# Kernel tuning notes

Measured on AMD Instinct MI355X. Metric: run time of the kernel, lower is better.

Reference implementation:

```python
import jax, jax.numpy as jnp
import numpy as np

B, S, E, H = 2, 2048, 2048, 16
D = E // H  # head_dim = 128
MASKED_BIAS = -1e9


def setup_inputs() -> dict:
    key = jax.random.key(0)
    ks = jax.random.split(key, 5)
    scale = 0.02
    return {
        "hidden_states": jax.random.normal(ks[0], (B, S, E), dtype=jnp.float32),
        "Wq": jax.random.normal(ks[1], (E, E), dtype=jnp.float32) * scale,
        "Wk": jax.random.normal(ks[2], (E, E), dtype=jnp.float32) * scale,
        "Wv": jax.random.normal(ks[3], (E, E), dtype=jnp.float32) * scale,
        "Wo": jax.random.normal(ks[4], (E, E), dtype=jnp.float32) * scale,
        "bo": jnp.zeros((E,), dtype=jnp.float32),
    }


def reference(hidden_states, Wq, Wk, Wv, Wo, bo):
    x = hidden_states
    # torch Linear: y = x @ W.T (no bias for q/k/v)
    q = jnp.einsum("bse,fe->bsf", x, Wq).reshape(B, S, H, D).transpose(0, 2, 1, 3)
    k = jnp.einsum("bse,fe->bsf", x, Wk).reshape(B, S, H, D).transpose(0, 2, 1, 3)
    v = jnp.einsum("bse,fe->bsf", x, Wv).reshape(B, S, H, D).transpose(0, 2, 1, 3)
    # GPT-Neo: NO 1/sqrt(d) scaling, attention computed in fp32
    scores = jnp.einsum("bhqd,bhkd->bhqk", q.astype(jnp.float32), k.astype(jnp.float32))
    causal = jnp.tril(jnp.ones((S, S), dtype=bool))[None, None]
    scores = jnp.where(causal, scores, jnp.float32(MASKED_BIAS))
    weights = jax.nn.softmax(scores, axis=-1).astype(v.dtype)
    attn = jnp.einsum("bhqk,bhkd->bhqd", weights, v)
    attn = attn.transpose(0, 2, 1, 3).reshape(B, S, E)
    out = jnp.einsum("bse,fe->bsf", attn, Wo) + bo
    return out
```

## Files before the change

### kernel.cpp

```cpp
#include <hip/hip_runtime.h>
#include <stdint.h>
#include <stddef.h>

#define Bd 2
#define Sd 2048
#define Ed 2048
#define Hd 16
#define Dd 128

typedef unsigned short u16;
typedef _Float16 f16;
typedef __attribute__((ext_vector_type(8))) _Float16 half8;
typedef __attribute__((ext_vector_type(4))) float f32x4;

__device__ __forceinline__ u16 f2h(float f) {
  f16 h = (f16)f; return __builtin_bit_cast(u16, h);
}
__device__ __forceinline__ void gll16(const void* g, void* lds) {
  __builtin_amdgcn_global_load_lds(
      (const __attribute__((address_space(1))) void*)g,
      (__attribute__((address_space(3))) void*)lds, 16, 0, 0);
}
template<int C> __device__ __forceinline__ float dppmv(float x) {
  return __builtin_bit_cast(float,
      __builtin_amdgcn_update_dpp(0, __builtin_bit_cast(int, x), C, 0xF, 0xF, false));
}
__device__ __forceinline__ float rmax16(float x) {
  x = fmaxf(x, dppmv<0x121>(x)); x = fmaxf(x, dppmv<0x122>(x));
  x = fmaxf(x, dppmv<0x124>(x)); x = fmaxf(x, dppmv<0x128>(x));
  return x;
}
__device__ __forceinline__ float rsum16(float x) {
  x += dppmv<0x121>(x); x += dppmv<0x122>(x);
  x += dppmv<0x124>(x); x += dppmv<0x128>(x);
  return x;
}
#define MFMA(a,b,c) __builtin_amdgcn_mfma_f32_16x16x32_f16((a),(b),(c),0,0,0)

#define BARRIER() do { __builtin_amdgcn_s_barrier(); __builtin_amdgcn_sched_barrier(0); } while (0)
#define LGKM(n) do { asm volatile("s_waitcnt lgkmcnt(" #n ")" ::: "memory"); __builtin_amdgcn_sched_barrier(0); } while (0)
#define VMCNT(n) do { asm volatile("s_waitcnt vmcnt(" #n ")" ::: "memory"); __builtin_amdgcn_sched_barrier(0); } while (0)

__global__ void k_cvt5(const float* __restrict__ x,
                       const float* __restrict__ Wq, const float* __restrict__ Wk,
                       const float* __restrict__ Wv, const float* __restrict__ Wo,
                       u16* __restrict__ xh, u16* __restrict__ wq, u16* __restrict__ wk,
                       u16* __restrict__ wv, u16* __restrict__ wo) {
  const int stride = gridDim.x * blockDim.x;
  for (int i = blockIdx.x * blockDim.x + threadIdx.x; i < 6291456; i += stride) {
    const float* s; u16* d; int j;
    if (i < 2097152) { s = x; d = xh; j = i; }
    else {
      const int t = (i - 2097152) >> 20;
      j = (i - 2097152) & 1048575;
      s = (t == 0) ? Wq : (t == 1) ? Wk : (t == 2) ? Wv : Wo;
      d = (t == 0) ? wq : (t == 1) ? wk : (t == 2) ? wv : wo;
    }
    const float4 v = ((const float4*)s)[j];
    ((ushort4*)d)[j] = make_ushort4(f2h(v.x), f2h(v.y), f2h(v.z), f2h(v.w));
  }
}

__global__ __launch_bounds__(512, 2) void gemm_qk(
    const u16* __restrict__ xh,
    const u16* __restrict__ wq, const u16* __restrict__ wk,
    u16* __restrict__ Qf, u16* __restrict__ Kf) {
  constexpr int NT = 32;
  __shared__ __align__(16) char smem[131072];
  const int lin = blockIdx.x;
  const int z = lin >> 7;
  const int rr = lin & 127;
  const int n0 = (rr & 7) * 256;
  const int m0 = (rr >> 3) * 256;
  const u16* wgt = z ? wk : wq;
  u16* oq = z ? Kf : Qf;
  const int tid = threadIdx.x, wv = tid >> 6, ln = tid & 63;
  const int wvm = wv >> 2, wvn = wv & 3;

  auto stgA = [&](int tt, int par) {
    if (tt >= NT) return;
    const int kin = tt << 6;
    const int c = tt & 1;
    const int r8 = ln >> 3, cc = ((ln & 7) ^ r8) * 16;
#pragma unroll
    for (int e = 0; e < 2; ++e) {
      const int ch = e * 8 + wv;
      const int trow = (par + (ch >> 3) * 2) * 64 + (ch & 7) * 8;
      gll16((const char*)xh + (size_t)(m0 + trow + r8) * 4096 + (size_t)kin * 2 + cc,
            smem + c * 65536 + trow * 128);
    }
  };
  auto stgB = [&](int tt, int n2) {
    if (tt >= NT) return;
    const int kin = tt << 6;
    const int c = tt & 1;
    const int r8 = ln >> 3, cc = ((ln & 7) ^ r8) * 16;
#pragma unroll
    for (int e = 0; e < 2; ++e) {
      const int ch = e * 8 + wv;
      const int trow = (ch >> 2) * 64 + n2 * 32 + (ch & 3) * 8;
      gll16((const char*)wgt + (size_t)(n0 + trow + r8) * 4096 + (size_t)kin * 2 + cc,
            smem + c * 65536 + 32768 + trow * 128);
    }
  };
  auto ldAh = [&](int c, int h, half8 (*a)[2]) {
#pragma unroll
    for (int mm = 0; mm < 4; ++mm) {
      const int row = wvm * 128 + h * 64 + mm * 16 + (ln & 15);
#pragma unroll
      for (int s = 0; s < 2; ++s) {
        const int cb = (s * 64 + (ln >> 4) * 16) ^ ((row & 7) << 4);
        a[mm][s] = *(const half8*)(smem + c * 65536 + row * 128 + cb);
      }
    }
  };
  auto ldBh = [&](int c, int n2, half8 (*b)[2]) {
#pragma unroll
    for (int nn = 0; nn < 2; ++nn) {
      const int row = wvn * 64 + (n2 * 2 + nn) * 16 + (ln & 15);
#pragma unroll
      for (int s = 0; s < 2; ++s) {
        const int cb = (s * 64 + (ln >> 4) * 16) ^ ((row & 7) << 4);
        b[nn][s] = *(const half8*)(smem + c * 65536 + 32768 + row * 128 + cb);
      }
    }
  };

  const f32x4 fz = {0.f, 0.f, 0.f, 0.f};
  f32x4 acc[8][4];
#pragma unroll
  for (int mm = 0; mm < 8; ++mm)
#pragma unroll
    for (int nn = 0; nn < 4; ++nn) acc[mm][nn] = fz;

#define QUAD(MB, NB, AA, BB)                                                    \
  do {                                                                          \
    __builtin_amdgcn_s_setprio(1);                                              \
    _Pragma("unroll")                                                           \
    for (int mm = 0; mm < 4; ++mm)                                              \
      _Pragma("unroll")                                                         \
      for (int nn = 0; nn < 2; ++nn) {                                          \
        acc[MB + mm][NB + nn] = MFMA(AA[mm][0], BB[nn][0], acc[MB + mm][NB + nn]); \
        acc[MB + mm][NB + nn] = MFMA(AA[mm][1], BB[nn][1], acc[MB + mm][NB + nn]); \
      }                                                                         \
    __builtin_amdgcn_s_setprio(0);                                              \
  } while (0)

  stgA(0, 0); stgA(0, 1); stgB(0, 0); stgB(0, 1);
  stgA(1, 0); stgB(1, 0); stgB(1, 1);
  VMCNT(6);
  BARRIER();

  for (int w = 0; w < NT; ++w) {
    const int c = w & 1;
    half8 a[4][2], b0[2][2], b1[2][2];
    ldAh(c, 0, a);
    ldBh(c, 0, b0);
    stgA(w + 1, 1);
    BARRIER(); LGKM(0);
    QUAD(0, 0, a, b0);
    BARRIER();
    ldBh(c, 1, b1);
    stgA(w + 2, 0);
    BARRIER(); LGKM(0);
    QUAD(0, 2, a, b1);
    BARRIER();
    ldAh(c, 1, a);
    stgB(w + 2, 0);
    BARRIER(); LGKM(0);
    QUAD(4, 0, a, b0);
    BARRIER();
    stgB(w + 2, 1);
    BARRIER();
    QUAD(4, 2, a, b1);
    if (w + 2 < NT) { VMCNT(6); } else { VMCNT(0); }
    BARRIER();
  }
#undef QUAD

#pragma unroll
  for (int mm = 0; mm < 8; ++mm)
#pragma unroll
    for (int nn = 0; nn < 4; ++nn)
#pragma unroll
      for (int r4 = 0; r4 < 4; ++r4) {
        const int mg = m0 + wvm * 128 + mm * 16 + (ln >> 4) * 4 + r4;
        const int f = n0 + wvn * 64 + nn * 16 + (ln & 15);
        const int b = mg >> 11, s = mg & (Sd - 1);
        const int h = f >> 7, d = f & (Dd - 1);
        oq[(((size_t)b * Hd + h) * Sd + s) * Dd + d] = f2h(acc[mm][nn][r4]);
      }
}

template<int MODE>
__global__ __launch_bounds__(512, 2) void gemm1(
    const u16* __restrict__ Ap, const u16* __restrict__ Bp,
    const float* __restrict__ bias, u16* __restrict__ ob, float* __restrict__ of) {
  constexpr int NT = 32;
  __shared__ __align__(16) char smem[98304];
  const int bid = blockIdx.x;
  const int n0 = (bid & 7) * 256;
  const int m0 = (bid >> 3) * 128;
  const int tid = threadIdx.x, wv = tid >> 6, ln = tid & 63;
  const int wvm = wv >> 2, wvn = wv & 3;

  auto stageA = [&](int tt, int c) {
    const int kin = tt << 6;
#pragma unroll
    for (int i = 0; i < 2; ++i) {
      const int l2 = i * 8192 + wv * 1024 + ln * 16;
      const int row = l2 >> 7, cb = l2 & 127;
      const int gc = cb ^ ((row & 7) << 4);
      gll16((const char*)Ap + (size_t)(m0 + row) * 4096 + (size_t)kin * 2 + gc,
            smem + c * 49152 + i * 8192 + wv * 1024);
    }
  };
  auto stageB = [&](int tt, int c) {
    const int kin = tt << 6;
#pragma unroll
    for (int i = 0; i < 4; ++i) {
      const int l2 = i * 8192 + wv * 1024 + ln * 16;
      const int row = l2 >> 7, cb = l2 & 127;
      const int gc = cb ^ ((row & 7) << 4);
      gll16((const char*)Bp + (size_t)(n0 + row) * 4096 + (size_t)kin * 2 + gc,
            smem + c * 49152 + 16384 + i * 8192 + wv * 1024);
    }
  };
  auto ldA = [&](int c, int s, half8* af) {
#pragma unroll
    for (int mm = 0; mm < 4; ++mm) {
      const int row = wvm * 64 + mm * 16 + (ln & 15);
      const int cb = (s * 64 + (ln >> 4) * 16) ^ ((row & 7) << 4);
      af[mm] = *(const half8*)(smem + c * 49152 + row * 128 + cb);
    }
  };
  auto ldB = [&](int c, int s, int p, half8* bf) {
#pragma unroll
    for (int j = 0; j < 2; ++j) {
      const int row = wvn * 64 + (p * 2 + j) * 16 + (ln & 15);
      const int cb = (s * 64 + (ln >> 4) * 16) ^ ((row & 7) << 4);
      bf[j] = *(const half8*)(smem + c * 49152 + 16384 + row * 128 + cb);
    }
  };

  const f32x4 fz = {0.f, 0.f, 0.f, 0.f};
  f32x4 acc[4][4];
#pragma unroll
  for (int mm = 0; mm < 4; ++mm)
#pragma unroll
    for (int nn = 0; nn < 4; ++nn) acc[mm][nn] = fz;

  stageA(0, 0);
  stageB(0, 0);
  stageA(1, 1);
  VMCNT(2);
  BARRIER();

  for (int t = 0; t < NT; ++t) {
    const int c = t & 1;
    const bool h1 = (t + 1 < NT), h2 = (t + 2 < NT);
    half8 af[4], bf01[2], bf23[2];
    ldA(c, 0, af);
    ldB(c, 0, 0, bf01);
    ldB(c, 0, 1, bf23);
    if (h1) stageB(t + 1, c ^ 1);
    BARRIER();
    LGKM(2);
    __builtin_amdgcn_s_setprio(1);
#pragma unroll
    for (int mm = 0; mm < 4; ++mm) {
      acc[mm][0] = MFMA(af[mm], bf01[0], acc[mm][0]);
      acc[mm][1] = MFMA(af[mm], bf01[1], acc[mm][1]);
    }
    __builtin_amdgcn_s_setprio(0);
    BARRIER();
    LGKM(0);
    __builtin_amdgcn_s_setprio(1);
#pragma unroll
    for (int mm = 0; mm < 4; ++mm) {
      acc[mm][2] = MFMA(af[mm], bf23[0], acc[mm][2]);
      acc[mm][3] = MFMA(af[mm], bf23[1], acc[mm][3]);
    }
    __builtin_amdgcn_s_setprio(0);
    BARRIER();
    ldA(c, 1, af);
    ldB(c, 1, 0, bf01);
    ldB(c, 1, 1, bf23);
    BARRIER();
    LGKM(2);
    __builtin_amdgcn_s_setprio(1);
#pragma unroll
    for (int mm = 0; mm < 4; ++mm) {
      acc[mm][0] = MFMA(af[mm], bf01[0], acc[mm][0]);
      acc[mm][1] = MFMA(af[mm], bf01[1], acc[mm][1]);
    }
    __builtin_amdgcn_s_setprio(0);
    BARRIER();
    if (h2) stageA(t + 2, c);
    LGKM(0);
    __builtin_amdgcn_s_setprio(1);
#pragma unroll
    for (int mm = 0; mm < 4; ++mm) {
      acc[mm][2] = MFMA(af[mm], bf23[0], acc[mm][2]);
      acc[mm][3] = MFMA(af[mm], bf23[1], acc[mm][3]);
    }
    __builtin_amdgcn_s_setprio(0);
    if (h2)      { VMCNT(2); }
    else if (h1) { VMCNT(0); }
    BARRIER();
  }

#pragma unroll
  for (int mm = 0; mm < 4; ++mm)
#pragma unroll
    for (int nn = 0; nn < 4; ++nn) {
      const int f = n0 + wvn * 64 + nn * 16 + (ln & 15);
      float bi = 0.f;
      if (MODE == 1) bi = bias[f];
#pragma unroll
      for (int r4 = 0; r4 < 4; ++r4) {
        const int mg = m0 + wvm * 64 + mm * 16 + (ln >> 4) * 4 + r4;
        if (MODE == 0) {
          const int b = mg >> 11, s = mg & (Sd - 1);
          const int h = f >> 7, d = f & (Dd - 1);
          ob[(((size_t)b * Hd + h) * Sd + s) * Dd + d] = f2h(acc[mm][nn][r4]);
        } else {
          of[(size_t)mg * Ed + f] = acc[mm][nn][r4] + bi;
        }
      }
    }
}

__global__ __launch_bounds__(256, 2) void k_attn(
    const u16* __restrict__ Qf, const u16* __restrict__ Kf,
    const u16* __restrict__ Vb, u16* __restrict__ ctx) {
  __shared__ __align__(16) char smem[53248];
  char* KsB = smem;
  char* VtB = smem + 16384;
  char* PlB = smem + 34816;

  const int bh = blockIdx.x;
  const int y = blockIdx.y;
  const int qt = (y < 8) ? y : (23 - y);
  const int tid = threadIdx.x, wv = tid >> 6, ln = tid & 63;
  const int q0 = qt * 128 + wv * 32;
  const size_t headoff = (size_t)bh * Sd * Dd;

  half8 qf[2][4];
#pragma unroll
  for (int mi = 0; mi < 2; ++mi)
#pragma unroll
    for (int c = 0; c < 4; ++c) {
      const size_t off = headoff + (size_t)(q0 + mi * 16 + (ln & 15)) * Dd + c * 32 + (ln >> 4) * 8;
      qf[mi][c] = *(const half8*)(Qf + off);
    }

  const f32x4 fz = {0.f, 0.f, 0.f, 0.f};
  f32x4 acc_o[2][8];
  float m_run[2][4], l_run[2][4];
#pragma unroll
  for (int mi = 0; mi < 2; ++mi) {
#pragma unroll
    for (int n = 0; n < 8; ++n) acc_o[mi][n] = fz;
#pragma unroll
    for (int r = 0; r < 4; ++r) { m_run[mi][r] = -1e30f; l_run[mi][r] = 0.f; }
  }

  const int ktmax = 2 * qt + 1;
  for (int kt = 0; kt <= ktmax; ++kt) {
    const size_t ktile = (headoff + (size_t)kt * 64 * Dd) * 2;
#pragma unroll
    for (int i = 0; i < 4; ++i) {
      const int lin = i * 4096 + wv * 1024 + ln * 16;
      const int row = lin >> 8;
      const int cb = lin & 255;
      const int gc = cb ^ ((row & 7) << 4);
      gll16((const char*)Kf + ktile + (size_t)row * 256 + gc, KsB + i * 4096 + wv * 1024);
    }
#pragma unroll
    for (int p = 0; p < 4; ++p) {
      const int rr = (tid >> 4) + 16 * p;
      const int d0 = (tid & 15) * 8;
      const ushort4 vv0 = *(const ushort4*)(Vb + headoff + (size_t)(kt * 64 + rr) * Dd + d0);
      const ushort4 vv1 = *(const ushort4*)(Vb + headoff + (size_t)(kt * 64 + rr) * Dd + d0 + 4);
      const u16 vs[8] = {vv0.x, vv0.y, vv0.z, vv0.w, vv1.x, vv1.y, vv1.z, vv1.w};
#pragma unroll
      for (int j = 0; j < 8; ++j) {
        const int d = d0 + j;
        *(u16*)(VtB + d * 144 + ((rr * 2) ^ (((d >> 3) & 7) << 4))) = vs[j];
      }
    }
    __syncthreads();

    const bool skip = (kt * 64) > (q0 + 31);

    f32x4 sc[2][4];
#pragma unroll
    for (int mi = 0; mi < 2; ++mi)
#pragma unroll
      for (int t = 0; t < 4; ++t) sc[mi][t] = fz;
    if (!skip) {
#pragma unroll
      for (int t = 0; t < 4; ++t)
#pragma unroll
        for (int c = 0; c < 4; ++c) {
          const int row = t * 16 + (ln & 15);
          const int cb = (c * 64 + (ln >> 4) * 16) ^ ((row & 7) << 4);
          const half8 kh8 = *(const half8*)(KsB + row * 256 + cb);
#pragma unroll
          for (int mi = 0; mi < 2; ++mi)
            sc[mi][t] = MFMA(qf[mi][c], kh8, sc[mi][t]);
        }
      if (kt >= 2 * qt) {
#pragma unroll
        for (int mi = 0; mi < 2; ++mi)
#pragma unroll
          for (int t = 0; t < 4; ++t)
#pragma unroll
            for (int r = 0; r < 4; ++r) {
              const int qg = q0 + mi * 16 + (ln >> 4) * 4 + r;
              const int kg = kt * 64 + t * 16 + (ln & 15);
              if (kg > qg) sc[mi][t][r] = -1e30f;
            }
      }

#pragma unroll
      for (int mi = 0; mi < 2; ++mi)
#pragma unroll
        for (int r = 0; r < 4; ++r) {
          float rm = fmaxf(fmaxf(sc[mi][0][r], sc[mi][1][r]),
                           fmaxf(sc[mi][2][r], sc[mi][3][r]));
          rm = rmax16(rm);
          const float mn = fmaxf(m_run[mi][r], rm);
          const float alpha = __expf(m_run[mi][r] - mn);
          m_run[mi][r] = mn;
          const int irow = mi * 16 + (ln >> 4) * 4 + r;
          float ps = 0.f;
#pragma unroll
          for (int t = 0; t < 4; ++t) {
            const float pv = __expf(sc[mi][t][r] - mn);
            ps += pv;
            *(u16*)(PlB + wv * 4608 + irow * 144 + (t * 16 + (ln & 15)) * 2) = f2h(pv);
          }
          ps = rsum16(ps);
          l_run[mi][r] = l_run[mi][r] * alpha + ps;
#pragma unroll
          for (int n = 0; n < 8; ++n) acc_o[mi][n][r] *= alpha;
        }
    }
    asm volatile("s_waitcnt lgkmcnt(0)" ::: "memory");
    __builtin_amdgcn_sched_barrier(0);

    if (!skip) {
      half8 pf[2][2];
#pragma unroll
      for (int mi = 0; mi < 2; ++mi)
#pragma unroll
        for (int c2 = 0; c2 < 2; ++c2)
          pf[mi][c2] = *(const half8*)(PlB + wv * 4608 + (mi * 16 + (ln & 15)) * 144 +
                                       c2 * 64 + (ln >> 4) * 16);
#pragma unroll
      for (int n = 0; n < 8; ++n)
#pragma unroll
        for (int c2 = 0; c2 < 2; ++c2) {
          const int d = n * 16 + (ln & 15);
          const half8 v8 = *(const half8*)(VtB + d * 144 +
                             ((c2 * 64 + (ln >> 4) * 16) ^ (((d >> 3) & 7) << 4)));
          acc_o[0][n] = MFMA(pf[0][c2], v8, acc_o[0][n]);
          acc_o[1][n] = MFMA(pf[1][c2], v8, acc_o[1][n]);
        }
    }
    __syncthreads();
  }

  const int b = bh >> 4, h = bh & 15;
#pragma unroll
  for (int mi = 0; mi < 2; ++mi)
#pragma unroll
    for (int r = 0; r < 4; ++r) {
      const float inv = 1.f / l_run[mi][r];
      const int s = q0 + mi * 16 + (ln >> 4) * 4 + r;
#pragma unroll
      for (int n = 0; n < 8; ++n) {
        const int col = n * 16 + (ln & 15);
        ctx[((size_t)b * Sd + s) * Ed + h * Dd + col] = f2h(acc_o[mi][n][r] * inv);
      }
    }
}

extern "C" void kernel_launch(void* const* d_in, const int* in_sizes, int n_in,
                              void* d_out, int out_size, void* d_ws, size_t ws_size,
                              hipStream_t stream) {
  (void)in_sizes; (void)n_in; (void)out_size; (void)ws_size;
  const float* x  = (const float*)d_in[0];
  const float* Wq = (const float*)d_in[1];
  const float* Wk = (const float*)d_in[2];
  const float* Wv = (const float*)d_in[3];
  const float* Wo = (const float*)d_in[4];
  const float* bo = (const float*)d_in[5];
  float* out = (float*)d_out;

  const size_t NTOK = (size_t)Bd * Sd * Ed;
  const size_t NW   = (size_t)Ed * Ed;

  char* w = (char*)d_ws;
  u16* xh  = (u16*)w; w += NTOK * 2;
  u16* wq  = (u16*)w; w += NW * 2;
  u16* wk  = (u16*)w; w += NW * 2;
  u16* wv  = (u16*)w; w += NW * 2;
  u16* wo  = (u16*)w; w += NW * 2;
  u16* Qf  = (u16*)w; w += NTOK * 2;
  u16* Kf  = (u16*)w; w += NTOK * 2;
  u16* Vf  = (u16*)w; w += NTOK * 2;
  u16* ctx = (u16*)w; w += NTOK * 2;

  k_cvt5<<<dim3(2048), 256, 0, stream>>>(x, Wq, Wk, Wv, Wo, xh, wq, wk, wv, wo);

  gemm_qk<<<dim3(256), 512, 0, stream>>>(xh, wq, wk, Qf, Kf);
  gemm1<0><<<dim3(256), 512, 0, stream>>>(xh, wv, nullptr, Vf, nullptr);

  k_attn<<<dim3(Bd * Hd, Sd / 128), 256, 0, stream>>>(Qf, Kf, Vf, ctx);

  gemm1<1><<<dim3(256), 512, 0, stream>>>(ctx, wo, bo, nullptr, out);
}
```

Baseline: 259.6 us.

## Split long causal attention tiles across two blocks with a combine kernel

The upper eight query tiles of each head are now split along the key dimension into two halves handled by separate blocks. Each half writes unnormalized fp32 partial outputs plus running max and sum to workspace, and a new combine kernel merges them into ctx. The aim is to balance work per block under the causal mask and raise the block count from 512 to 768, with the occupancy hint raised from 2 to 3. In exchange it adds an extra kernel launch and fp32 partial-output traffic through global memory.

```diff
diff --git a/kernel.cpp b/kernel.cpp
--- a/kernel.cpp
+++ b/kernel.cpp
@@ -331,9 +331,10 @@
     }
 }
 
-__global__ __launch_bounds__(256, 2) void k_attn(
+__global__ __launch_bounds__(256, 3) void k_attn(
     const u16* __restrict__ Qf, const u16* __restrict__ Kf,
-    const u16* __restrict__ Vb, u16* __restrict__ ctx) {
+    const u16* __restrict__ Vb, u16* __restrict__ ctx,
+    float* __restrict__ Op, float* __restrict__ ml) {
   __shared__ __align__(16) char smem[53248];
   char* KsB = smem;
   char* VtB = smem + 16384;
@@ -341,7 +342,12 @@
 
   const int bh = blockIdx.x;
   const int y = blockIdx.y;
-  const int qt = (y < 8) ? y : (23 - y);
+  int qt, half;
+  if (y < 8)       { qt = 7 - y;  half = -1; }
+  else if (y < 16) { qt = y;      half = 0;  }
+  else             { qt = y - 8;  half = 1;  }
+  const int klo = (half == 1) ? (qt + 1) : 0;
+  const int khi = (half == 0) ? (qt + 1) : (2 * qt + 2);
   const int tid = threadIdx.x, wv = tid >> 6, ln = tid & 63;
   const int q0 = qt * 128 + wv * 32;
   const size_t headoff = (size_t)bh * Sd * Dd;
@@ -366,8 +372,7 @@
     for (int r = 0; r < 4; ++r) { m_run[mi][r] = -1e30f; l_run[mi][r] = 0.f; }
   }
 
-  const int ktmax = 2 * qt + 1;
-  for (int kt = 0; kt <= ktmax; ++kt) {
+  for (int kt = klo; kt < khi; ++kt) {
     const size_t ktile = (headoff + (size_t)kt * 64 * Dd) * 2;
 #pragma unroll
     for (int i = 0; i < 4; ++i) {
@@ -473,19 +478,71 @@
     __syncthreads();
   }
 
+  if (half < 0) {
+    const int b = bh >> 4, h = bh & 15;
+#pragma unroll
+    for (int mi = 0; mi < 2; ++mi)
+#pragma unroll
+      for (int r = 0; r < 4; ++r) {
+        const float inv = 1.f / l_run[mi][r];
+        const int s = q0 + mi * 16 + (ln >> 4) * 4 + r;
+#pragma unroll
+        for (int n = 0; n < 8; ++n) {
+          const int col = n * 16 + (ln & 15);
+          ctx[((size_t)b * Sd + s) * Ed + h * Dd + col] = f2h(acc_o[mi][n][r] * inv);
+        }
+      }
+  } else {
+    const int tile = bh * 8 + (qt - 8);
+    const int pi = tile * 2 + half;
+    const size_t ob = (size_t)pi * 16384;
+#pragma unroll
+    for (int mi = 0; mi < 2; ++mi)
+#pragma unroll
+      for (int r = 0; r < 4; ++r) {
+        const int row = wv * 32 + mi * 16 + (ln >> 4) * 4 + r;
+        if ((ln & 15) == 0) {
+          ml[((size_t)pi * 128 + row) * 2 + 0] = m_run[mi][r];
+          ml[((size_t)pi * 128 + row) * 2 + 1] = l_run[mi][r];
+        }
+#pragma unroll
+        for (int n = 0; n < 8; ++n)
+          Op[ob + (size_t)row * 128 + n * 16 + (ln & 15)] = acc_o[mi][n][r];
+      }
+  }
+}
+
+__global__ __launch_bounds__(256) void k_comb(const float* __restrict__ Op,
+                                              const float* __restrict__ ml,
+                                              u16* __restrict__ ctx) {
+  const int t = blockIdx.x;
+  const int bh = t >> 3;
+  const int qt = 8 + (t & 7);
   const int b = bh >> 4, h = bh & 15;
-#pragma unroll
-  for (int mi = 0; mi < 2; ++mi)
-#pragma unroll
-    for (int r = 0; r < 4; ++r) {
-      const float inv = 1.f / l_run[mi][r];
-      const int s = q0 + mi * 16 + (ln >> 4) * 4 + r;
-#pragma unroll
-      for (int n = 0; n < 8; ++n) {
-        const int col = n * 16 + (ln & 15);
-        ctx[((size_t)b * Sd + s) * Ed + h * Dd + col] = f2h(acc_o[mi][n][r] * inv);
-      }
-    }
+  const int tid = threadIdx.x;
+  const int row = tid >> 1;
+  const int d0 = (tid & 1) * 64;
+  const float m1 = ml[((size_t)(t * 2 + 0) * 128 + row) * 2 + 0];
+  const float l1 = ml[((size_t)(t * 2 + 0) * 128 + row) * 2 + 1];
+  const float m2 = ml[((size_t)(t * 2 + 1) * 128 + row) * 2 + 0];
+  const float l2 = ml[((size_t)(t * 2 + 1) * 128 + row) * 2 + 1];
+  const float m = fmaxf(m1, m2);
+  const float w1 = __expf(m1 - m), w2 = __expf(m2 - m);
+  const float inv = 1.f / (w1 * l1 + w2 * l2);
+  const float a1 = w1 * inv, a2 = w2 * inv;
+  const size_t o1 = (size_t)(t * 2 + 0) * 16384 + (size_t)row * 128 + d0;
+  const size_t o2 = (size_t)(t * 2 + 1) * 16384 + (size_t)row * 128 + d0;
+  const int s = qt * 128 + row;
+  u16* co = ctx + ((size_t)b * Sd + s) * Ed + h * Dd + d0;
+#pragma unroll
+  for (int j = 0; j < 16; ++j) {
+    const float4 u = *(const float4*)(Op + o1 + j * 4);
+    const float4 v = *(const float4*)(Op + o2 + j * 4);
+    co[j * 4 + 0] = f2h(a1 * u.x + a2 * v.x);
+    co[j * 4 + 1] = f2h(a1 * u.y + a2 * v.y);
+    co[j * 4 + 2] = f2h(a1 * u.z + a2 * v.z);
+    co[j * 4 + 3] = f2h(a1 * u.w + a2 * v.w);
+  }
 }
 
 extern "C" void kernel_launch(void* const* d_in, const int* in_sizes, int n_in,
@@ -513,13 +570,16 @@
   u16* Kf  = (u16*)w; w += NTOK * 2;
   u16* Vf  = (u16*)w; w += NTOK * 2;
   u16* ctx = (u16*)w; w += NTOK * 2;
+  float* Op = (float*)w; w += (size_t)512 * 16384 * 4;
+  float* ml = (float*)w; w += (size_t)512 * 128 * 2 * 4;
 
   k_cvt5<<<dim3(2048), 256, 0, stream>>>(x, Wq, Wk, Wv, Wo, xh, wq, wk, wv, wo);
 
   gemm_qk<<<dim3(256), 512, 0, stream>>>(xh, wq, wk, Qf, Kf);
   gemm1<0><<<dim3(256), 512, 0, stream>>>(xh, wv, nullptr, Vf, nullptr);
 
-  k_attn<<<dim3(Bd * Hd, Sd / 128), 256, 0, stream>>>(Qf, Kf, Vf, ctx);
+  k_attn<<<dim3(Bd * Hd, 24), 256, 0, stream>>>(Qf, Kf, Vf, ctx, Op, ml);
+  k_comb<<<dim3(256), 256, 0, stream>>>(Op, ml, ctx);
 
   gemm1<1><<<dim3(256), 512, 0, stream>>>(ctx, wo, bo, nullptr, out);
 }
```

New measurement: 334.8 us. 29.0% more time.

## Pack V transpose stores and add lazy softmax rescaling in attention

Applied to the files above, without the earlier changes.

The V tile transpose into LDS now loads four consecutive rows per thread with 16-byte loads and writes packed 8-byte stores instead of scalar 2-byte stores. This cuts LDS store instruction count. The online softmax also skips the rescale of the running max and accumulator unless some row's new max exceeds the old one by more than a threshold, checked by a wave-wide ballot. This avoids the alpha exponentials and accumulator multiplies on most tiles, at the cost of exponent values up to e^8 in fp16 probabilities. The grid change from Sd/128 to 16 keeps the same value.

```diff
diff --git a/kernel.cpp b/kernel.cpp
--- a/kernel.cpp
+++ b/kernel.cpp
@@ -366,6 +366,9 @@
     for (int r = 0; r < 4; ++r) { m_run[mi][r] = -1e30f; l_run[mi][r] = 0.f; }
   }
 
+  const int q4 = tid >> 4;
+  const int dg = tid & 15;
+
   const int ktmax = 2 * qt + 1;
   for (int kt = 0; kt <= ktmax; ++kt) {
     const size_t ktile = (headoff + (size_t)kt * 64 * Dd) * 2;
@@ -377,17 +380,18 @@
       const int gc = cb ^ ((row & 7) << 4);
       gll16((const char*)Kf + ktile + (size_t)row * 256 + gc, KsB + i * 4096 + wv * 1024);
     }
-#pragma unroll
-    for (int p = 0; p < 4; ++p) {
-      const int rr = (tid >> 4) + 16 * p;
-      const int d0 = (tid & 15) * 8;
-      const ushort4 vv0 = *(const ushort4*)(Vb + headoff + (size_t)(kt * 64 + rr) * Dd + d0);
-      const ushort4 vv1 = *(const ushort4*)(Vb + headoff + (size_t)(kt * 64 + rr) * Dd + d0 + 4);
-      const u16 vs[8] = {vv0.x, vv0.y, vv0.z, vv0.w, vv1.x, vv1.y, vv1.z, vv1.w};
+    {
+      union { uint4 u; u16 h[8]; } vr[4];
+#pragma unroll
+      for (int i = 0; i < 4; ++i)
+        vr[i].u = *(const uint4*)(Vb + headoff + (size_t)(kt * 64 + q4 * 4 + i) * Dd + dg * 8);
 #pragma unroll
       for (int j = 0; j < 8; ++j) {
-        const int d = d0 + j;
-        *(u16*)(VtB + d * 144 + ((rr * 2) ^ (((d >> 3) & 7) << 4))) = vs[j];
+        const int d = dg * 8 + j;
+        const uint32_t lo = (uint32_t)vr[0].h[j] | ((uint32_t)vr[1].h[j] << 16);
+        const uint32_t hi = (uint32_t)vr[2].h[j] | ((uint32_t)vr[3].h[j] << 16);
+        uint2 pk; pk.x = lo; pk.y = hi;
+        *(uint2*)(VtB + d * 144 + ((q4 * 8) ^ (((d >> 3) & 7) << 4))) = pk;
       }
     }
     __syncthreads();
@@ -424,6 +428,8 @@
             }
       }
 
+      float rm_[2][4];
+      bool flag = false;
 #pragma unroll
       for (int mi = 0; mi < 2; ++mi)
 #pragma unroll
@@ -431,22 +437,48 @@
           float rm = fmaxf(fmaxf(sc[mi][0][r], sc[mi][1][r]),
                            fmaxf(sc[mi][2][r], sc[mi][3][r]));
           rm = rmax16(rm);
-          const float mn = fmaxf(m_run[mi][r], rm);
-          const float alpha = __expf(m_run[mi][r] - mn);
-          m_run[mi][r] = mn;
-          const int irow = mi * 16 + (ln >> 4) * 4 + r;
-          float ps = 0.f;
-#pragma unroll
-          for (int t = 0; t < 4; ++t) {
-            const float pv = __expf(sc[mi][t][r] - mn);
-            ps += pv;
-            *(u16*)(PlB + wv * 4608 + irow * 144 + (t * 16 + (ln & 15)) * 2) = f2h(pv);
+          rm_[mi][r] = rm;
+          flag |= (rm > m_run[mi][r] + 8.f);
+        }
+      if (__ballot(flag) != 0ull) {
+#pragma unroll
+        for (int mi = 0; mi < 2; ++mi)
+#pragma unroll
+          for (int r = 0; r < 4; ++r) {
+            const float mn = fmaxf(m_run[mi][r], rm_[mi][r]);
+            const float alpha = __expf(m_run[mi][r] - mn);
+            m_run[mi][r] = mn;
+            const int irow = mi * 16 + (ln >> 4) * 4 + r;
+            float ps = 0.f;
+#pragma unroll
+            for (int t = 0; t < 4; ++t) {
+              const float pv = __expf(sc[mi][t][r] - mn);
+              ps += pv;
+              *(u16*)(PlB + wv * 4608 + irow * 144 + (t * 16 + (ln & 15)) * 2) = f2h(pv);
+            }
+            ps = rsum16(ps);
+            l_run[mi][r] = l_run[mi][r] * alpha + ps;
+#pragma unroll
+            for (int n = 0; n < 8; ++n) acc_o[mi][n][r] *= alpha;
           }
-          ps = rsum16(ps);
-          l_run[mi][r] = l_run[mi][r] * alpha + ps;
-#pragma unroll
-          for (int n = 0; n < 8; ++n) acc_o[mi][n][r] *= alpha;
-        }
+      } else {
+#pragma unroll
+        for (int mi = 0; mi < 2; ++mi)
+#pragma unroll
+          for (int r = 0; r < 4; ++r) {
+            const float mn = m_run[mi][r];
+            const int irow = mi * 16 + (ln >> 4) * 4 + r;
+            float ps = 0.f;
+#pragma unroll
+            for (int t = 0; t < 4; ++t) {
+              const float pv = __expf(sc[mi][t][r] - mn);
+              ps += pv;
+              *(u16*)(PlB + wv * 4608 + irow * 144 + (t * 16 + (ln & 15)) * 2) = f2h(pv);
+            }
+            ps = rsum16(ps);
+            l_run[mi][r] += ps;
+          }
+      }
     }
     asm volatile("s_waitcnt lgkmcnt(0)" ::: "memory");
     __builtin_amdgcn_sched_barrier(0);
@@ -519,7 +551,7 @@
   gemm_qk<<<dim3(256), 512, 0, stream>>>(xh, wq, wk, Qf, Kf);
   gemm1<0><<<dim3(256), 512, 0, stream>>>(xh, wv, nullptr, Vf, nullptr);
 
-  k_attn<<<dim3(Bd * Hd, Sd / 128), 256, 0, stream>>>(Qf, Kf, Vf, ctx);
+  k_attn<<<dim3(Bd * Hd, 16), 256, 0, stream>>>(Qf, Kf, Vf, ctx);
 
   gemm1<1><<<dim3(256), 512, 0, stream>>>(ctx, wo, bo, nullptr, out);
 }
```

Measured after the change: 280.9 us. 8.2% more time.
